# Optimization experiments

Hardware: AMD Instinct MI355X
Metric: run time of the kernel (lower is better)

Reference implementation:

```python
import jax, jax.numpy as jnp
import numpy as np
from jax import lax

B, L = 2, 1024
D_MODEL, D_STATE, EXPAND, D_CONV = 1024, 16, 2, 4
D_INNER = EXPAND * D_MODEL            # 2048
DT_RANK = (D_MODEL + 15) // 16        # 64


def setup_inputs() -> dict:
    key = jax.random.key(0)
    ks = jax.random.split(key, 8)
    g = lambda k, shape, s=0.02: jax.random.normal(k, shape, dtype=jnp.float32) * s
    # Mamba-style A init: A = -exp(A_log), A_log = log(1..d_state) per channel
    A_log = jnp.log(jnp.broadcast_to(
        jnp.arange(1, D_STATE + 1, dtype=jnp.float32), (D_INNER, D_STATE)))
    return {
        "x": jax.random.normal(ks[0], (B, L, D_MODEL), dtype=jnp.float32),
        "W_in": g(ks[1], (D_MODEL, 2 * D_INNER)),
        "conv_w": g(ks[2], (D_INNER, D_CONV), 0.1),
        "conv_b": jnp.zeros((D_INNER,), jnp.float32),
        "W_x": g(ks[3], (D_INNER, DT_RANK + 2 * D_STATE)),
        "W_dt": g(ks[4], (DT_RANK, D_INNER)),
        "b_dt": g(ks[5], (D_INNER,), 0.1),
        "A_log": A_log,
        "D_skip": jnp.ones((D_INNER,), jnp.float32),
        "W_out": g(ks[6], (D_INNER, D_MODEL)),
    }


def reference(x, W_in, conv_w, conv_b, W_x, W_dt, b_dt, A_log, D_skip, W_out):
    # in_proj -> (u, z): [B, L, D_INNER] each
    xz = x @ W_in
    u, z = xz[..., :D_INNER], xz[..., D_INNER:]

    # causal depthwise conv1d, kernel D_CONV (small fixed loop over taps)
    up = jnp.pad(u, ((0, 0), (D_CONV - 1, 0), (0, 0)))
    u = sum(up[:, k:k + L, :] * conv_w[:, k] for k in range(D_CONV)) + conv_b
    u = jax.nn.silu(u)

    # input-dependent dt, B, C
    x_dbl = u @ W_x                                    # [B, L, dt_rank + 2N]
    dt = x_dbl[..., :DT_RANK]
    Bm = x_dbl[..., DT_RANK:DT_RANK + D_STATE]         # [B, L, N]
    Cm = x_dbl[..., DT_RANK + D_STATE:]                # [B, L, N]
    delta = jax.nn.softplus(dt @ W_dt + b_dt)          # [B, L, D]

    A = -jnp.exp(A_log)                                # [D, N]
    deltaA = jnp.exp(jnp.einsum('bld,dn->bldn', delta, A))   # [B, L, D, N]
    dBu = (delta * u)[..., None] * Bm[:, :, None, :]          # [B, L, D, N]

    def step(h, inp):
        dA_t, dBu_t, c_t = inp                         # [B,D,N],[B,D,N],[B,N]
        h = dA_t * h + dBu_t
        y_t = jnp.einsum('bdn,bn->bd', h, c_t)
        return h, y_t

    h0 = jnp.zeros((B, D_INNER, D_STATE), x.dtype)
    _, ys = lax.scan(step, h0,
                     (deltaA.transpose(1, 0, 2, 3),
                      dBu.transpose(1, 0, 2, 3),
                      Cm.transpose(1, 0, 2)))
    y = ys.transpose(1, 0, 2) + u * D_skip             # [B, L, D_INNER]
    y = y * jax.nn.silu(z)                             # gated output
    return y @ W_out                                   # [B, L, D_MODEL]
```

## Files before the change

### kernel.cpp

```cpp
#include <hip/hip_runtime.h>


typedef unsigned short u16;
typedef unsigned int   u32;

#define B_SZ 2
#define L_SZ 1024
#define DM   1024
#define DI   2048
#define DS   16
#define DTR  64
#define NXD  96
#define NCHUNK 32
#define CL   32
#define KSPLIT 8
#define KC     256

typedef __bf16 bf16x8 __attribute__((ext_vector_type(8)));
typedef float  f32x4  __attribute__((ext_vector_type(4)));

__device__ __forceinline__ u16 f2bf(float f) {
    u32 x = __float_as_uint(f);
    x += 0x7fffu + ((x >> 16) & 1u);
    return (u16)(x >> 16);
}
__device__ __forceinline__ float bf2f(u16 v) {
    return __uint_as_float(((u32)v) << 16);
}

__device__ __forceinline__ void gld_lds16(const u16* g, u16* l) {
    __builtin_amdgcn_global_load_lds(
        (const __attribute__((address_space(1))) u32*)g,
        (__attribute__((address_space(3))) u32*)l, 16, 0, 0);
}

__device__ __forceinline__ void wg_barrier() {
    __asm__ volatile("" ::: "memory");
    __builtin_amdgcn_s_barrier();
    __asm__ volatile("" ::: "memory");
}
#define WAIT_VM12() __builtin_amdgcn_s_waitcnt(0xF7C)
#define WAIT_VM8()  __builtin_amdgcn_s_waitcnt(0xF78)
#define WAIT_VM6()  __builtin_amdgcn_s_waitcnt(0xF76)
#define WAIT_VM4()  __builtin_amdgcn_s_waitcnt(0xF74)
#define WAIT_VM2()  __builtin_amdgcn_s_waitcnt(0xF72)
#define WAIT_VM0()  __builtin_amdgcn_s_waitcnt(0xF70)

__global__ __launch_bounds__(256) void gemm128p(
    const u16* __restrict__ A, const u16* __restrict__ BT,
    float* __restrict__ Cf, u16* __restrict__ Cb,
    int M, int N, int K, int op)
{
    __shared__ u16 As[4][128 * 32];
    __shared__ u16 Bs[4][128 * 32];

    const int tid  = threadIdx.x;
    const int wave = tid >> 6;
    const int lane = tid & 63;
    const int q    = lane >> 4;
    const int r16  = lane & 15;
    const int wm   = (wave & 1) * 64;
    const int wn   = (wave >> 1) * 64;
    const int flat = blockIdx.y * 32 + blockIdx.x;
    const int xcd  = flat & 7;
    const int idx  = flat >> 3;
    const int m0   = (idx >> 2) * 128;
    const int n0   = (xcd * 4 + (idx & 3)) * 128;

    const u16* gA0 = A  + (size_t)(m0 + (tid >> 2))      * K + (tid & 3) * 8;
    const u16* gA1 = A  + (size_t)(m0 + 64 + (tid >> 2)) * K + (tid & 3) * 8;
    const u16* gB0 = BT + (size_t)(n0 + (tid >> 2))      * K + (tid & 3) * 8;
    const u16* gB1 = BT + (size_t)(n0 + 64 + (tid >> 2)) * K + (tid & 3) * 8;

    const int niter = K >> 5;
    const int pre = niter < 3 ? niter : 3;
    for (int p = 0; p < pre; ++p) {
        const int k0 = p * 32;
        gld_lds16(gA0 + k0, &As[p][tid * 8]);
        gld_lds16(gA1 + k0, &As[p][2048 + tid * 8]);
        gld_lds16(gB0 + k0, &Bs[p][tid * 8]);
        gld_lds16(gB1 + k0, &Bs[p][2048 + tid * 8]);
    }

    f32x4 acc[4][4];
#pragma unroll
    for (int s = 0; s < 4; ++s)
#pragma unroll
        for (int j = 0; j < 4; ++j) acc[s][j] = (f32x4){0.f, 0.f, 0.f, 0.f};

    for (int it = 0; it < niter; ++it) {
        if (it + 3 < niter) {
            const int k0 = (it + 3) * 32;
            const int bi = (it + 3) & 3;
            gld_lds16(gA0 + k0, &As[bi][tid * 8]);
            gld_lds16(gA1 + k0, &As[bi][2048 + tid * 8]);
            gld_lds16(gB0 + k0, &Bs[bi][tid * 8]);
            gld_lds16(gB1 + k0, &Bs[bi][2048 + tid * 8]);
            WAIT_VM12();
        } else if (it + 2 < niter) {
            WAIT_VM8();
        } else if (it + 1 < niter) {
            WAIT_VM4();
        } else {
            WAIT_VM0();
        }
        wg_barrier();

        const int cur = it & 3;
        bf16x8 af[4], bfr[4];
#pragma unroll
        for (int s = 0; s < 4; ++s)
            af[s] = *(const bf16x8*)(&As[cur][(wm + s * 16 + r16) * 32 + q * 8]);
#pragma unroll
        for (int j = 0; j < 4; ++j)
            bfr[j] = *(const bf16x8*)(&Bs[cur][(wn + j * 16 + r16) * 32 + q * 8]);
#pragma unroll
        for (int s = 0; s < 4; ++s)
#pragma unroll
            for (int j = 0; j < 4; ++j)
                acc[s][j] = __builtin_amdgcn_mfma_f32_16x16x32_bf16(
                    af[s], bfr[j], acc[s][j], 0, 0, 0);

        wg_barrier();
    }

#pragma unroll
    for (int s = 0; s < 4; ++s) {
        const int row0 = m0 + wm + s * 16 + q * 4;
#pragma unroll
        for (int j = 0; j < 4; ++j) {
            const int col = n0 + wn + j * 16 + r16;
            if (op == 2) {
#pragma unroll
                for (int i = 0; i < 4; ++i)
                    Cb[(size_t)(row0 + i) * N + col] = f2bf(acc[s][j][i]);
            } else {
#pragma unroll
                for (int i = 0; i < 4; ++i)
                    Cf[(size_t)(row0 + i) * N + col] = acc[s][j][i];
            }
        }
    }
}

__global__ __launch_bounds__(256) void gemm_out64(
    const u16* __restrict__ A, const u16* __restrict__ BT,
    float* __restrict__ C, int M, int N, int K)
{
    __shared__ u16 As[4][64 * 32];
    __shared__ u16 Bs[4][64 * 32];

    const int tid  = threadIdx.x;
    const int wave = tid >> 6;
    const int lane = tid & 63;
    const int q    = lane >> 4;
    const int r16  = lane & 15;
    const int wm   = (wave & 1) * 32;
    const int wn   = (wave >> 1) * 32;
    const int flat = blockIdx.y * 16 + blockIdx.x;
    const int xcd  = flat & 7;
    const int idx  = flat >> 3;
    const int n0   = (xcd * 2 + (idx & 1)) * 64;
    const int m0   = (idx >> 1) * 64;

    const u16* gA0 = A  + (size_t)(m0 + (tid >> 2)) * K + (tid & 3) * 8;
    const u16* gB0 = BT + (size_t)(n0 + (tid >> 2)) * K + (tid & 3) * 8;

    const int niter = K >> 5;
    const int pre = niter < 3 ? niter : 3;
    for (int p = 0; p < pre; ++p) {
        const int k0 = p * 32;
        gld_lds16(gA0 + k0, &As[p][tid * 8]);
        gld_lds16(gB0 + k0, &Bs[p][tid * 8]);
    }

    f32x4 acc[2][2];
#pragma unroll
    for (int s = 0; s < 2; ++s)
#pragma unroll
        for (int j = 0; j < 2; ++j) acc[s][j] = (f32x4){0.f, 0.f, 0.f, 0.f};

    for (int it = 0; it < niter; ++it) {
        if (it + 3 < niter) {
            const int k0 = (it + 3) * 32;
            const int bi = (it + 3) & 3;
            gld_lds16(gA0 + k0, &As[bi][tid * 8]);
            gld_lds16(gB0 + k0, &Bs[bi][tid * 8]);
            WAIT_VM6();
        } else if (it + 2 < niter) {
            WAIT_VM4();
        } else if (it + 1 < niter) {
            WAIT_VM2();
        } else {
            WAIT_VM0();
        }
        wg_barrier();

        const int cur = it & 3;
        bf16x8 af[2], bfr[2];
#pragma unroll
        for (int s = 0; s < 2; ++s)
            af[s] = *(const bf16x8*)(&As[cur][(wm + s * 16 + r16) * 32 + q * 8]);
#pragma unroll
        for (int j = 0; j < 2; ++j)
            bfr[j] = *(const bf16x8*)(&Bs[cur][(wn + j * 16 + r16) * 32 + q * 8]);
#pragma unroll
        for (int s = 0; s < 2; ++s)
#pragma unroll
            for (int j = 0; j < 2; ++j)
                acc[s][j] = __builtin_amdgcn_mfma_f32_16x16x32_bf16(
                    af[s], bfr[j], acc[s][j], 0, 0, 0);

        wg_barrier();
    }

#pragma unroll
    for (int s = 0; s < 2; ++s) {
        const int row0 = m0 + wm + s * 16 + q * 4;
#pragma unroll
        for (int j = 0; j < 2; ++j) {
            const int col = n0 + wn + j * 16 + r16;
#pragma unroll
            for (int i = 0; i < 4; ++i)
                C[(size_t)(row0 + i) * N + col] = acc[s][j][i];
        }
    }
}

__global__ __launch_bounds__(256) void gemm_skinny_conv(
    const u16* __restrict__ xzbf, const float* __restrict__ cw,
    const float* __restrict__ cb, const u16* __restrict__ BT,
    float* xdbl, u16* __restrict__ ucbf)
{
    constexpr int LDT = 40;
    __shared__ u16 As[128 * LDT];
    __shared__ u16 Bs[64 * LDT];

    const int tid  = threadIdx.x;
    const int wave = tid >> 6;
    const int lane = tid & 63;
    const int q    = lane >> 4;
    const int r16  = lane & 15;
    const int m0   = blockIdx.y * 128;
    const int n0   = blockIdx.x * 64;
    const int kcs  = blockIdx.z * KC;
    const int sr   = tid >> 2;
    const int ss   = (tid & 3) * 8;

    f32x4 acc[2][4];
#pragma unroll
    for (int s = 0; s < 2; ++s)
#pragma unroll
        for (int j = 0; j < 4; ++j) acc[s][j] = (f32x4){0.f, 0.f, 0.f, 0.f};

    const int bcol  = n0 + sr;
    const int bcolc = bcol < NXD ? bcol : NXD - 1;

    constexpr int NIT = KC / 32;
    for (int it = 0; it < NIT; ++it) {
        const int c = kcs + it * 32 + ss;
        __syncthreads();

        f32x4 cwv[8];
        float cbv[8];
#pragma unroll
        for (int j = 0; j < 8; ++j) {
            cwv[j] = *(const f32x4*)(cw + (size_t)(c + j) * 4);
            cbv[j] = cb[c + j];
        }

        uint4 ua[2];
#pragma unroll
        for (int rsel = 0; rsel < 2; ++rsel) {
            const int r = m0 + rsel * 64 + sr;
            const int l = r & (L_SZ - 1);
            float s8[8];
#pragma unroll
            for (int j = 0; j < 8; ++j) s8[j] = cbv[j];
#pragma unroll
            for (int k = 0; k < 4; ++k) {
                if (l + k - 3 >= 0) {
                    uint4 xv = *(const uint4*)(xzbf + (size_t)(r + k - 3) * (2 * DI) + c);
                    const u16* xp = (const u16*)&xv;
#pragma unroll
                    for (int j = 0; j < 8; ++j) {
                        const float w = (k == 0) ? cwv[j].x : (k == 1) ? cwv[j].y
                                       : (k == 2) ? cwv[j].z : cwv[j].w;
                        s8[j] = fmaf(bf2f(xp[j]), w, s8[j]);
                    }
                }
            }
            u16* up = (u16*)&ua[rsel];
#pragma unroll
            for (int j = 0; j < 8; ++j) {
                float v = s8[j] / (1.f + __expf(-s8[j]));
                up[j] = f2bf(v);
            }
        }
        *(uint4*)(As + sr * LDT + ss)        = ua[0];
        *(uint4*)(As + (64 + sr) * LDT + ss) = ua[1];
        if (n0 == 0) {
            *(uint4*)(ucbf + (size_t)(m0 + sr) * DI + c)      = ua[0];
            *(uint4*)(ucbf + (size_t)(m0 + 64 + sr) * DI + c) = ua[1];
        }
        *(uint4*)(Bs + sr * LDT + ss) =
            *(const uint4*)(BT + (size_t)bcolc * DI + kcs + it * 32 + ss);
        __syncthreads();

        bf16x8 af[2], bfr[4];
#pragma unroll
        for (int s = 0; s < 2; ++s)
            af[s] = *(const bf16x8*)(As + (wave * 32 + s * 16 + r16) * LDT + q * 8);
#pragma unroll
        for (int j = 0; j < 4; ++j)
            bfr[j] = *(const bf16x8*)(Bs + (j * 16 + r16) * LDT + q * 8);
#pragma unroll
        for (int s = 0; s < 2; ++s)
#pragma unroll
            for (int j = 0; j < 4; ++j)
                acc[s][j] = __builtin_amdgcn_mfma_f32_16x16x32_bf16(
                    af[s], bfr[j], acc[s][j], 0, 0, 0);
    }

#pragma unroll
    for (int s = 0; s < 2; ++s) {
        const int row0 = m0 + wave * 32 + s * 16 + q * 4;
#pragma unroll
        for (int j = 0; j < 4; ++j) {
            const int col = n0 + j * 16 + r16;
            if (col < NXD) {
#pragma unroll
                for (int i = 0; i < 4; ++i)
                    atomicAdd(&xdbl[(size_t)(row0 + i) * NXD + col], acc[s][j][i]);
            }
        }
    }
}

__device__ __forceinline__ void tr_tile(
    const float* __restrict__ in, u16* __restrict__ out,
    int R, int C, int tr, int tc, int tid, float (*t)[33])
{
    const int tx = tid & 31, ty = tid >> 5;
    const int r0 = tr * 32, c0 = tc * 32;
#pragma unroll
    for (int i = 0; i < 4; ++i) {
        int r = r0 + ty + i * 8, c = c0 + tx;
        if (r < R && c < C) t[ty + i * 8][tx] = in[(size_t)r * C + c];
    }
    __syncthreads();
#pragma unroll
    for (int i = 0; i < 4; ++i) {
        int oR = c0 + ty + i * 8, oC = r0 + tx;
        if (oR < C && oC < R) out[(size_t)oR * R + oC] = f2bf(t[tx][ty + i * 8]);
    }
}

__global__ __launch_bounds__(256) void prep_kernel(
    const float* __restrict__ x,     u16* __restrict__ xbf,
    const float* __restrict__ W_in,  u16* __restrict__ winT,
    const float* __restrict__ W_out, u16* __restrict__ woutT,
    const float* __restrict__ W_x,   u16* __restrict__ wxT,
    const float* __restrict__ W_dt,  u16* __restrict__ wdtT,
    float* __restrict__ xdbl)
{
    __shared__ float t[32][33];
    const int id  = blockIdx.x;
    const int tid = threadIdx.x;
    if (id < 4096) {
        tr_tile(W_in, winT, 1024, 4096, id >> 7, id & 127, tid, t);
    } else if (id < 6144) {
        int i2 = id - 4096;
        tr_tile(W_out, woutT, 2048, 1024, i2 >> 5, i2 & 31, tid, t);
    } else if (id < 6336) {
        int i3 = id - 6144;
        tr_tile(W_x, wxT, 2048, 96, i3 / 3, i3 % 3, tid, t);
    } else if (id < 6464) {
        int i4 = id - 6336;
        tr_tile(W_dt, wdtT, 64, 2048, i4 >> 6, i4 & 63, tid, t);
    } else if (id < 14656) {
        int i = (id - 6464) * 256 + tid;
        xbf[i] = f2bf(x[i]);
    } else {
        f32x4 z = (f32x4){0.f, 0.f, 0.f, 0.f};
        ((f32x4*)xdbl)[(size_t)(id - 14656) * 256 + tid] = z;
    }
}

__device__ __forceinline__ void compute_delta_tile(
    const float* __restrict__ xdbl, const u16* __restrict__ wdtT,
    const float* __restrict__ b_dt, int rowbase, int d0, int tid,
    float (*dl)[256])
{
    const int wave = tid >> 6;
    const int lane = tid & 63;
    const int q    = lane >> 4;
    const int r16  = lane & 15;

    f32x4 dacc[2][4];
#pragma unroll
    for (int mt = 0; mt < 2; ++mt)
#pragma unroll
        for (int nt = 0; nt < 4; ++nt) dacc[mt][nt] = (f32x4){0.f, 0.f, 0.f, 0.f};

#pragma unroll
    for (int ks = 0; ks < 2; ++ks) {
        bf16x8 afr[2];
#pragma unroll
        for (int mt = 0; mt < 2; ++mt) {
            const float* ap = xdbl + (size_t)(rowbase + mt * 16 + r16) * NXD + ks * 32 + q * 8;
            f32x4 a0 = *(const f32x4*)ap;
            f32x4 a1 = *(const f32x4*)(ap + 4);
            union { u16 u[8]; bf16x8 v; } cvt;
#pragma unroll
            for (int i = 0; i < 4; ++i) { cvt.u[i] = f2bf(a0[i]); cvt.u[4 + i] = f2bf(a1[i]); }
            afr[mt] = cvt.v;
        }
#pragma unroll
        for (int nt = 0; nt < 4; ++nt) {
            const u16* bp = wdtT + (size_t)(d0 + (wave * 4 + nt) * 16 + r16) * DTR + ks * 32 + q * 8;
            bf16x8 bfr = *(const bf16x8*)bp;
#pragma unroll
            for (int mt = 0; mt < 2; ++mt)
                dacc[mt][nt] = __builtin_amdgcn_mfma_f32_16x16x32_bf16(
                    afr[mt], bfr, dacc[mt][nt], 0, 0, 0);
        }
    }

#pragma unroll
    for (int mt = 0; mt < 2; ++mt)
#pragma unroll
        for (int nt = 0; nt < 4; ++nt) {
            const int colg = (wave * 4 + nt) * 16 + r16;
            const float bv = b_dt[d0 + colg];
#pragma unroll
            for (int i = 0; i < 4; ++i) {
                float v = dacc[mt][nt][i] + bv;
                v = (v > 20.f) ? v : log1pf(__expf(v));
                dl[mt * 16 + q * 4 + i][colg] = v;
            }
        }
}

__global__ __launch_bounds__(256) void scan_pass1(
    const u16* __restrict__ ucbf, const float* __restrict__ xdbl,
    const u16* __restrict__ wdtT, const float* __restrict__ b_dt,
    const float* __restrict__ A_log,
    float* __restrict__ hbuf, float* __restrict__ pbuf)
{
    __shared__ float dl[CL][256];
    const int c = blockIdx.x;
    const int g = blockIdx.y;
    const int b = blockIdx.z;
    const int tid = threadIdx.x;
    const int d = g * 256 + tid;
    const int rowbase = b * L_SZ + c * CL;

    compute_delta_tile(xdbl, wdtT, b_dt, rowbase, g * 256, tid, dl);
    __syncthreads();

    float Av[16], h[16], P[16];
#pragma unroll
    for (int n = 0; n < 16; ++n) {
        Av[n] = -__expf(A_log[d * 16 + n]);
        h[n] = 0.f; P[n] = 1.f;
    }
    for (int i = 0; i < CL; ++i) {
        const int row = rowbase + i;
        float dlt = dl[i][tid];
        float uu  = bf2f(ucbf[(size_t)row * DI + d]);
        float du  = dlt * uu;
        const float* xr = xdbl + (size_t)row * NXD;
#pragma unroll
        for (int n = 0; n < 16; ++n) {
            float e = __expf(dlt * Av[n]);
            P[n] *= e;
            h[n] = fmaf(e, h[n], du * xr[DTR + n]);
        }
    }
    size_t base = ((size_t)((b * NCHUNK + c) * DI + d)) * 16;
#pragma unroll
    for (int n = 0; n < 16; ++n) { hbuf[base + n] = h[n]; pbuf[base + n] = P[n]; }
}

__global__ __launch_bounds__(256) void scan_pass2(
    float* __restrict__ hbuf, const float* __restrict__ pbuf)
{
    const int j = blockIdx.x * 256 + threadIdx.x;
    const int b = blockIdx.y;
    float h0 = 0.f;
    for (int cc = 0; cc < NCHUNK; ++cc) {
        size_t o = ((size_t)(b * NCHUNK + cc)) * (DI * 16) + j;
        float hl = hbuf[o];
        float Pl = pbuf[o];
        hbuf[o] = h0;
        h0 = fmaf(Pl, h0, hl);
    }
}

__global__ __launch_bounds__(256) void scan_pass3(
    const u16* __restrict__ ucbf, const float* __restrict__ xdbl,
    const u16* __restrict__ wdtT, const float* __restrict__ b_dt,
    const float* __restrict__ A_log, const float* __restrict__ hbuf,
    const u16* __restrict__ xzbf, const float* __restrict__ Dskip,
    u16* __restrict__ ybf)
{
    __shared__ float dl[CL][256];
    const int c = blockIdx.x;
    const int g = blockIdx.y;
    const int b = blockIdx.z;
    const int tid = threadIdx.x;
    const int d = g * 256 + tid;
    const int rowbase = b * L_SZ + c * CL;

    compute_delta_tile(xdbl, wdtT, b_dt, rowbase, g * 256, tid, dl);
    __syncthreads();

    float Av[16], h[16];
    size_t base = ((size_t)((b * NCHUNK + c) * DI + d)) * 16;
#pragma unroll
    for (int n = 0; n < 16; ++n) {
        Av[n] = -__expf(A_log[d * 16 + n]);
        h[n]  = hbuf[base + n];
    }
    const float Dk = Dskip[d];
    for (int i = 0; i < CL; ++i) {
        const int row = rowbase + i;
        float dlt = dl[i][tid];
        float uu  = bf2f(ucbf[(size_t)row * DI + d]);
        float du  = dlt * uu;
        const float* xr = xdbl + (size_t)row * NXD;
        float y = 0.f;
#pragma unroll
        for (int n = 0; n < 16; ++n) {
            float e = __expf(dlt * Av[n]);
            h[n] = fmaf(e, h[n], du * xr[DTR + n]);
            y = fmaf(h[n], xr[DTR + DS + n], y);
        }
        float zz = bf2f(xzbf[(size_t)row * (2 * DI) + DI + d]);
        float yv = fmaf(uu, Dk, y) * (zz / (1.f + __expf(-zz)));
        ybf[(size_t)row * DI + d] = f2bf(yv);
    }
}

constexpr size_t OFF_XDBL    = 0;
constexpr size_t OFF_HBUF    = OFF_XDBL + 196608;
constexpr size_t OFF_PBUF    = OFF_HBUF + 2097152;
constexpr size_t OFF_F32_END = OFF_PBUF + 2097152;
constexpr size_t SOFF_XBF   = 0;
constexpr size_t SOFF_WINT  = SOFF_XBF   + 2097152;
constexpr size_t SOFF_XZBF  = SOFF_WINT  + 4194304;
constexpr size_t SOFF_UCBF  = SOFF_XZBF  + 8388608;
constexpr size_t SOFF_WXT   = SOFF_UCBF  + 4194304;
constexpr size_t SOFF_WDTT  = SOFF_WXT   + 196608;
constexpr size_t SOFF_WOUTT = SOFF_WDTT  + 131072;
constexpr size_t SOFF_YBF   = SOFF_WOUTT + 2097152;

extern "C" void kernel_launch(void* const* d_in, const int* in_sizes, int n_in,
                              void* d_out, int out_size, void* d_ws, size_t ws_size,
                              hipStream_t stream)
{
    const float* x     = (const float*)d_in[0];
    const float* W_in  = (const float*)d_in[1];
    const float* cw    = (const float*)d_in[2];
    const float* cb    = (const float*)d_in[3];
    const float* W_x   = (const float*)d_in[4];
    const float* W_dt  = (const float*)d_in[5];
    const float* b_dt  = (const float*)d_in[6];
    const float* A_log = (const float*)d_in[7];
    const float* Dsk   = (const float*)d_in[8];
    const float* W_out = (const float*)d_in[9];
    float* out = (float*)d_out;

    float* wsf   = (float*)d_ws;
    float* xdbl  = wsf + OFF_XDBL;
    float* hbuf  = wsf + OFF_HBUF;
    float* pbuf  = wsf + OFF_PBUF;
    u16* sb    = (u16*)(wsf + OFF_F32_END);
    u16* xbf   = sb + SOFF_XBF;
    u16* winT  = sb + SOFF_WINT;
    u16* xzbf  = sb + SOFF_XZBF;
    u16* ucbf  = sb + SOFF_UCBF;
    u16* wxT   = sb + SOFF_WXT;
    u16* wdtT  = sb + SOFF_WDTT;
    u16* woutT = sb + SOFF_WOUTT;
    u16* ybf   = sb + SOFF_YBF;

    prep_kernel<<<14848, 256, 0, stream>>>(x, xbf, W_in, winT, W_out, woutT,
                                           W_x, wxT, W_dt, wdtT, xdbl);

    gemm128p<<<dim3(32, 16), 256, 0, stream>>>(
        xbf, winT, nullptr, xzbf, 2048, 4096, 1024, 2);

    gemm_skinny_conv<<<dim3(2, 16, KSPLIT), 256, 0, stream>>>(
        xzbf, cw, cb, wxT, xdbl, ucbf);

    scan_pass1<<<dim3(NCHUNK, DI / 256, B_SZ), 256, 0, stream>>>(
        ucbf, xdbl, wdtT, b_dt, A_log, hbuf, pbuf);
    scan_pass2<<<dim3(DI * 16 / 256, B_SZ), 256, 0, stream>>>(hbuf, pbuf);
    scan_pass3<<<dim3(NCHUNK, DI / 256, B_SZ), 256, 0, stream>>>(
        ucbf, xdbl, wdtT, b_dt, A_log, hbuf, xzbf, Dsk, ybf);

    gemm_out64<<<dim3(16, 32), 256, 0, stream>>>(ybf, woutT, out, 2048, 1024, 2048);
}
```

Baseline: 270.3 us.

## Halve scan chunk length and software-prefetch next-row scan inputs

Doubles the number of scan chunks (chunk length 16 instead of 32), giving more blocks for the two chunked scan passes. The delta tile computation drops to a single 16-row MFMA tile to match. Both passes now load the next row's u, z, B and C values into registers one iteration early, hiding global-load latency in the sequential recurrence. The cost is doubled h/P carry buffers and a longer sequential pass2 over chunks.

```diff
diff --git a/kernel.cpp b/kernel.cpp
--- a/kernel.cpp
+++ b/kernel.cpp
@@ -11,8 +11,8 @@
 #define DS   16
 #define DTR  64
 #define NXD  96
-#define NCHUNK 32
-#define CL   32
+#define NCHUNK 64
+#define CL   16
 #define KSPLIT 8
 #define KC     256
 
@@ -397,49 +397,38 @@
     const int q    = lane >> 4;
     const int r16  = lane & 15;
 
-    f32x4 dacc[2][4];
-#pragma unroll
-    for (int mt = 0; mt < 2; ++mt)
-#pragma unroll
-        for (int nt = 0; nt < 4; ++nt) dacc[mt][nt] = (f32x4){0.f, 0.f, 0.f, 0.f};
+    f32x4 dacc[4];
+#pragma unroll
+    for (int nt = 0; nt < 4; ++nt) dacc[nt] = (f32x4){0.f, 0.f, 0.f, 0.f};
 
 #pragma unroll
     for (int ks = 0; ks < 2; ++ks) {
-        bf16x8 afr[2];
-#pragma unroll
-        for (int mt = 0; mt < 2; ++mt) {
-            const float* ap = xdbl + (size_t)(rowbase + mt * 16 + r16) * NXD + ks * 32 + q * 8;
-            f32x4 a0 = *(const f32x4*)ap;
-            f32x4 a1 = *(const f32x4*)(ap + 4);
-            union { u16 u[8]; bf16x8 v; } cvt;
-#pragma unroll
-            for (int i = 0; i < 4; ++i) { cvt.u[i] = f2bf(a0[i]); cvt.u[4 + i] = f2bf(a1[i]); }
-            afr[mt] = cvt.v;
-        }
+        const float* ap = xdbl + (size_t)(rowbase + r16) * NXD + ks * 32 + q * 8;
+        f32x4 a0 = *(const f32x4*)ap;
+        f32x4 a1 = *(const f32x4*)(ap + 4);
+        union { u16 u[8]; bf16x8 v; } cvt;
+#pragma unroll
+        for (int i = 0; i < 4; ++i) { cvt.u[i] = f2bf(a0[i]); cvt.u[4 + i] = f2bf(a1[i]); }
 #pragma unroll
         for (int nt = 0; nt < 4; ++nt) {
             const u16* bp = wdtT + (size_t)(d0 + (wave * 4 + nt) * 16 + r16) * DTR + ks * 32 + q * 8;
             bf16x8 bfr = *(const bf16x8*)bp;
-#pragma unroll
-            for (int mt = 0; mt < 2; ++mt)
-                dacc[mt][nt] = __builtin_amdgcn_mfma_f32_16x16x32_bf16(
-                    afr[mt], bfr, dacc[mt][nt], 0, 0, 0);
-        }
-    }
-
-#pragma unroll
-    for (int mt = 0; mt < 2; ++mt)
-#pragma unroll
-        for (int nt = 0; nt < 4; ++nt) {
-            const int colg = (wave * 4 + nt) * 16 + r16;
-            const float bv = b_dt[d0 + colg];
-#pragma unroll
-            for (int i = 0; i < 4; ++i) {
-                float v = dacc[mt][nt][i] + bv;
-                v = (v > 20.f) ? v : log1pf(__expf(v));
-                dl[mt * 16 + q * 4 + i][colg] = v;
-            }
-        }
+            dacc[nt] = __builtin_amdgcn_mfma_f32_16x16x32_bf16(
+                cvt.v, bfr, dacc[nt], 0, 0, 0);
+        }
+    }
+
+#pragma unroll
+    for (int nt = 0; nt < 4; ++nt) {
+        const int colg = (wave * 4 + nt) * 16 + r16;
+        const float bv = b_dt[d0 + colg];
+#pragma unroll
+        for (int i = 0; i < 4; ++i) {
+            float v = dacc[nt][i] + bv;
+            v = (v > 20.f) ? v : log1pf(__expf(v));
+            dl[q * 4 + i][colg] = v;
+        }
+    }
 }
 
 __global__ __launch_bounds__(256) void scan_pass1(
@@ -465,17 +454,34 @@
         Av[n] = -__expf(A_log[d * 16 + n]);
         h[n] = 0.f; P[n] = 1.f;
     }
+
+    float un = bf2f(ucbf[(size_t)rowbase * DI + d]);
+    f32x4 bn0 = *(const f32x4*)(xdbl + (size_t)rowbase * NXD + DTR);
+    f32x4 bn1 = *(const f32x4*)(xdbl + (size_t)rowbase * NXD + DTR + 4);
+    f32x4 bn2 = *(const f32x4*)(xdbl + (size_t)rowbase * NXD + DTR + 8);
+    f32x4 bn3 = *(const f32x4*)(xdbl + (size_t)rowbase * NXD + DTR + 12);
+
     for (int i = 0; i < CL; ++i) {
-        const int row = rowbase + i;
-        float dlt = dl[i][tid];
-        float uu  = bf2f(ucbf[(size_t)row * DI + d]);
-        float du  = dlt * uu;
-        const float* xr = xdbl + (size_t)row * NXD;
+        const float uu = un;
+        const f32x4 b0 = bn0, b1 = bn1, b2 = bn2, b3 = bn3;
+        if (i + 1 < CL) {
+            const int rn = rowbase + i + 1;
+            un  = bf2f(ucbf[(size_t)rn * DI + d]);
+            const float* xr = xdbl + (size_t)rn * NXD;
+            bn0 = *(const f32x4*)(xr + DTR);
+            bn1 = *(const f32x4*)(xr + DTR + 4);
+            bn2 = *(const f32x4*)(xr + DTR + 8);
+            bn3 = *(const f32x4*)(xr + DTR + 12);
+        }
+        const float dlt = dl[i][tid];
+        const float du  = dlt * uu;
+        const float Bv[16] = {b0.x, b0.y, b0.z, b0.w, b1.x, b1.y, b1.z, b1.w,
+                              b2.x, b2.y, b2.z, b2.w, b3.x, b3.y, b3.z, b3.w};
 #pragma unroll
         for (int n = 0; n < 16; ++n) {
             float e = __expf(dlt * Av[n]);
             P[n] *= e;
-            h[n] = fmaf(e, h[n], du * xr[DTR + n]);
+            h[n] = fmaf(e, h[n], du * Bv[n]);
         }
     }
     size_t base = ((size_t)((b * NCHUNK + c) * DI + d)) * 16;
@@ -524,20 +530,50 @@
         h[n]  = hbuf[base + n];
     }
     const float Dk = Dskip[d];
+
+    float un = bf2f(ucbf[(size_t)rowbase * DI + d]);
+    float zn = bf2f(xzbf[(size_t)rowbase * (2 * DI) + DI + d]);
+    f32x4 bn0 = *(const f32x4*)(xdbl + (size_t)rowbase * NXD + DTR);
+    f32x4 bn1 = *(const f32x4*)(xdbl + (size_t)rowbase * NXD + DTR + 4);
+    f32x4 bn2 = *(const f32x4*)(xdbl + (size_t)rowbase * NXD + DTR + 8);
+    f32x4 bn3 = *(const f32x4*)(xdbl + (size_t)rowbase * NXD + DTR + 12);
+    f32x4 cn0 = *(const f32x4*)(xdbl + (size_t)rowbase * NXD + DTR + DS);
+    f32x4 cn1 = *(const f32x4*)(xdbl + (size_t)rowbase * NXD + DTR + DS + 4);
+    f32x4 cn2 = *(const f32x4*)(xdbl + (size_t)rowbase * NXD + DTR + DS + 8);
+    f32x4 cn3 = *(const f32x4*)(xdbl + (size_t)rowbase * NXD + DTR + DS + 12);
+
     for (int i = 0; i < CL; ++i) {
-        const int row = rowbase + i;
-        float dlt = dl[i][tid];
-        float uu  = bf2f(ucbf[(size_t)row * DI + d]);
-        float du  = dlt * uu;
-        const float* xr = xdbl + (size_t)row * NXD;
+        const float uu = un, zz = zn;
+        const f32x4 b0 = bn0, b1 = bn1, b2 = bn2, b3 = bn3;
+        const f32x4 c0 = cn0, c1 = cn1, c2 = cn2, c3 = cn3;
+        if (i + 1 < CL) {
+            const int rn = rowbase + i + 1;
+            un = bf2f(ucbf[(size_t)rn * DI + d]);
+            zn = bf2f(xzbf[(size_t)rn * (2 * DI) + DI + d]);
+            const float* xr = xdbl + (size_t)rn * NXD;
+            bn0 = *(const f32x4*)(xr + DTR);
+            bn1 = *(const f32x4*)(xr + DTR + 4);
+            bn2 = *(const f32x4*)(xr + DTR + 8);
+            bn3 = *(const f32x4*)(xr + DTR + 12);
+            cn0 = *(const f32x4*)(xr + DTR + DS);
+            cn1 = *(const f32x4*)(xr + DTR + DS + 4);
+            cn2 = *(const f32x4*)(xr + DTR + DS + 8);
+            cn3 = *(const f32x4*)(xr + DTR + DS + 12);
+        }
+        const float dlt = dl[i][tid];
+        const float du  = dlt * uu;
+        const float Bv[16] = {b0.x, b0.y, b0.z, b0.w, b1.x, b1.y, b1.z, b1.w,
+                              b2.x, b2.y, b2.z, b2.w, b3.x, b3.y, b3.z, b3.w};
+        const float Cv[16] = {c0.x, c0.y, c0.z, c0.w, c1.x, c1.y, c1.z, c1.w,
+                              c2.x, c2.y, c2.z, c2.w, c3.x, c3.y, c3.z, c3.w};
         float y = 0.f;
 #pragma unroll
         for (int n = 0; n < 16; ++n) {
             float e = __expf(dlt * Av[n]);
-            h[n] = fmaf(e, h[n], du * xr[DTR + n]);
-            y = fmaf(h[n], xr[DTR + DS + n], y);
-        }
-        float zz = bf2f(xzbf[(size_t)row * (2 * DI) + DI + d]);
+            h[n] = fmaf(e, h[n], du * Bv[n]);
+            y = fmaf(h[n], Cv[n], y);
+        }
+        const int row = rowbase + i;
         float yv = fmaf(uu, Dk, y) * (zz / (1.f + __expf(-zz)));
         ybf[(size_t)row * DI + d] = f2bf(yv);
     }
@@ -545,8 +581,8 @@
 
 constexpr size_t OFF_XDBL    = 0;
 constexpr size_t OFF_HBUF    = OFF_XDBL + 196608;
-constexpr size_t OFF_PBUF    = OFF_HBUF + 2097152;
-constexpr size_t OFF_F32_END = OFF_PBUF + 2097152;
+constexpr size_t OFF_PBUF    = OFF_HBUF + 4194304;
+constexpr size_t OFF_F32_END = OFF_PBUF + 4194304;
 constexpr size_t SOFF_XBF   = 0;
 constexpr size_t SOFF_WINT  = SOFF_XBF   + 2097152;
 constexpr size_t SOFF_XZBF  = SOFF_WINT  + 4194304;
```

Result: faster. 264.0 us (-2.3%).
